# Kernel tuning notes

Measured on AMD Instinct MI355X. Metric: run time of the kernel, lower is better.

Reference implementation:

```python
import jax, jax.numpy as jnp
import numpy as np

B, T, D, I, C, H = 8192, 128, 7, 128, 10, 64
L = 2 ** D
SUBSET = int(I * 0.8)  # feature_subset_size = 102


def setup_inputs() -> dict:
    key = jax.random.key(0)
    ks = jax.random.split(key, 7)
    x = jax.random.normal(ks[0], (B, I), dtype=jnp.float32)
    # exact feature-subset mask: SUBSET ones per (tree, depth) row
    r = jax.random.uniform(ks[1], (T, D, I))
    ranks = jnp.argsort(jnp.argsort(r, axis=-1), axis=-1)
    feature_mask = (ranks < SUBSET).astype(jnp.float32)
    thresholds = jax.random.normal(ks[2], (T, D), dtype=jnp.float32)
    leaf_outputs = jax.random.normal(ks[3], (T, L, C), dtype=jnp.float32)
    W1 = jax.random.normal(ks[4], (I, H), dtype=jnp.float32) * 0.08
    b1 = jnp.zeros((H,), dtype=jnp.float32)
    W2 = jax.random.normal(ks[5], (H, T), dtype=jnp.float32) * 0.12
    b2 = jnp.zeros((T,), dtype=jnp.float32)
    return {"x": x, "feature_mask": feature_mask, "thresholds": thresholds,
            "leaf_outputs": leaf_outputs, "W1": W1, "b1": b1, "W2": W2, "b2": b2}


def reference(x, feature_mask, thresholds, leaf_outputs, W1, b1, W2, b2):
    depth = thresholds.shape[1]
    # split logits: masked feature sum minus threshold, per (batch, tree, depth)
    z = jnp.einsum('bi,tdi->btd', x, feature_mask) - thresholds[None, :, :]
    s = 0.5 * (z / (1.0 + jnp.abs(z)) + 1.0)  # scaled softsign split in (0,1)
    # probabilistic path routing: doubling concat, identical to torch loop
    p = jnp.ones((x.shape[0], feature_mask.shape[0], 1), dtype=x.dtype)
    for d in range(depth):
        sd = s[:, :, d:d + 1]            # [B, T, 1]
        p = jnp.concatenate([p * sd, p * (1.0 - sd)], axis=-1)  # [B, T, 2^(d+1)]
    leaf_probs = jax.nn.softmax(leaf_outputs, axis=-1)           # [T, L, C]
    tree_outputs = jnp.einsum('btl,tlc->btc', p, leaf_probs)     # [B, T, C]
    # instance-wise attention over trees (eval mode: no dropout)
    attn = jax.nn.softmax(jax.nn.relu(x @ W1 + b1) @ W2 + b2, axis=-1)  # [B, T]
    return jnp.sum(tree_outputs * attn[:, :, None], axis=1)     # [B, C]
```

## Files before the change

kernel.cpp:

```cpp
#include <hip/hip_runtime.h>
#include <hip/hip_bf16.h>
#include <hip/hip_fp16.h>


#define BB 8192
#define TT 128
#define II 128
#define CC 10
#define HH 64

typedef __attribute__((ext_vector_type(8))) short short8;
typedef __attribute__((ext_vector_type(16))) float floatx16;

static __device__ inline unsigned int pkbf(float lo, float hi) {
  __hip_bfloat162 h = __float22bfloat162_rn(make_float2(lo, hi));
  unsigned int u;
  __builtin_memcpy(&u, &h, 4);
  return u;
}

static __device__ inline unsigned int pkh(float lo, float hi) {
  __half2 h = __float22half2_rn(make_float2(lo, hi));
  unsigned int u;
  __builtin_memcpy(&u, &h, 4);
  return u;
}

static __device__ inline short8 cvt8(float4 a, float4 b) {
  union { short8 v; unsigned int u[4]; } r;
  r.u[0] = pkbf(a.x, a.y);
  r.u[1] = pkbf(a.z, a.w);
  r.u[2] = pkbf(b.x, b.y);
  r.u[3] = pkbf(b.z, b.w);
  return r.v;
}

__global__ __launch_bounds__(256, 2) void fused_kernel(
    const float* __restrict__ x, const float* __restrict__ mask,
    const float* __restrict__ thr, const float* __restrict__ lo,
    const float* __restrict__ W1, const float* __restrict__ b1,
    const float* __restrict__ W2, const float* __restrict__ b2,
    float* __restrict__ out) {
  __shared__ __align__(16) char smem_raw[63488];
  const int tid = threadIdx.x;
  const int wv = tid >> 6, lane = tid & 63;
  const int half = lane >> 5, l31 = lane & 31;
  const int tg = blockIdx.x >> 5;
  const int bg = blockIdx.x & 31;

  __half* zsl = (__half*)smem_raw;

  {
    const int m0 = tg * 56;
    short8 af0[8], af1[8];
    {
      const float* mrow0 = mask + (size_t)(m0 + l31) * II + half * 8;
      int mr1 = m0 + 28 + l31; if (mr1 > 895) mr1 = 895;
      const float* mrow1 = mask + (size_t)mr1 * II + half * 8;
#pragma unroll
      for (int s = 0; s < 8; ++s) {
        af0[s] = cvt8(*(const float4*)(mrow0 + s * 16),
                      *(const float4*)(mrow0 + s * 16 + 4));
        af1[s] = cvt8(*(const float4*)(mrow1 + s * 16),
                      *(const float4*)(mrow1 + s * 16 + 4));
      }
    }
    float th0[16], th1[16];
#pragma unroll
    for (int r = 0; r < 16; ++r) {
      int rw = (r & 3) + 8 * (r >> 2) + 4 * half;
      th0[r] = thr[m0 + rw];
      int m1 = m0 + 28 + rw;
      th1[r] = thr[m1 > 895 ? 895 : m1];
    }

#pragma unroll
    for (int nb = 0; nb < 2; ++nb) {
      const int nl = wv * 64 + nb * 32;
      const float* xrow = x + (size_t)(bg * 256 + nl + l31) * II + half * 8;
      short8 xf[8];
#pragma unroll
      for (int s = 0; s < 8; ++s)
        xf[s] = cvt8(*(const float4*)(xrow + s * 16),
                     *(const float4*)(xrow + s * 16 + 4));
      floatx16 acc0, acc1;
#pragma unroll
      for (int i = 0; i < 16; ++i) { acc0[i] = 0.f; acc1[i] = 0.f; }
#pragma unroll
      for (int s = 0; s < 8; ++s) {
        acc0 = __builtin_amdgcn_mfma_f32_32x32x16_bf16(af0[s], xf[s], acc0, 0, 0, 0);
        acc1 = __builtin_amdgcn_mfma_f32_32x32x16_bf16(af1[s], xf[s], acc1, 0, 0, 0);
      }
#pragma unroll
      for (int r = 0; r < 16; ++r) {
        int row = (r & 3) + 8 * (r >> 2) + 4 * half;
        if (row < 28) {
          int tl = row / 7;
          int d = row - tl * 7;
          float z = acc0[r] - th0[r];
          float o = 0.5f * (z / (1.f + fabsf(z)) + 1.f);
          zsl[(tl * 256 + nl + l31) * 8 + d] = __float2half(o);
          z = acc1[r] - th1[r];
          o = 0.5f * (z / (1.f + fabsf(z)) + 1.f);
          zsl[((tl + 4) * 256 + nl + l31) * 8 + d] = __float2half(o);
        }
      }
    }
  }

  {
    const int tsel = tg >> 2, lsel = tg & 3;
    __half* attnV = (__half*)(smem_raw + 59392);
    for (int p = 0; p < 2; ++p) {
      const int b0 = bg * 256 + p * 128 + wv * 32;

      short8 axf[8];
      const float* xrow = x + (size_t)(b0 + l31) * II + half * 8;
#pragma unroll
      for (int s = 0; s < 8; ++s)
        axf[s] = cvt8(*(const float4*)(xrow + s * 16),
                      *(const float4*)(xrow + s * 16 + 4));

      floatx16 acch[2];
#pragma unroll
      for (int i = 0; i < 16; ++i) { acch[0][i] = 0.f; acch[1][i] = 0.f; }
#pragma unroll
      for (int s = 0; s < 8; ++s) {
#pragma unroll
        for (int tile = 0; tile < 2; ++tile) {
          union { short8 v; unsigned int u[4]; } wf;
#pragma unroll
          for (int jp = 0; jp < 4; ++jp) {
            int k0 = s * 16 + half * 8 + jp * 2;
            float f0 = W1[(size_t)k0 * HH + tile * 32 + l31];
            float f1 = W1[(size_t)(k0 + 1) * HH + tile * 32 + l31];
            wf.u[jp] = pkbf(f0, f1);
          }
          acch[tile] = __builtin_amdgcn_mfma_f32_32x32x16_bf16(
              axf[s], wf.v, acch[tile], 0, 0, 0);
        }
      }
      __hip_bfloat16* hids = (__hip_bfloat16*)(smem_raw + 32768) + wv * (32 * 72);
#pragma unroll
      for (int tile = 0; tile < 2; ++tile) {
        float bh = b1[tile * 32 + l31];
#pragma unroll
        for (int r = 0; r < 16; ++r) {
          int row = (r & 3) + 8 * (r >> 2) + 4 * half;
          hids[row * 72 + tile * 32 + l31] =
              __float2bfloat16(fmaxf(acch[tile][r] + bh, 0.f));
        }
      }
      __syncthreads();

      short8 ahf[4];
#pragma unroll
      for (int s = 0; s < 4; ++s)
        ahf[s] = *(const short8*)(hids + l31 * 72 + s * 16 + half * 8);

      floatx16 accl[4];
#pragma unroll
      for (int tile = 0; tile < 4; ++tile) {
#pragma unroll
        for (int i = 0; i < 16; ++i) accl[tile][i] = 0.f;
#pragma unroll
        for (int s = 0; s < 4; ++s) {
          union { short8 v; unsigned int u[4]; } wf;
#pragma unroll
          for (int jp = 0; jp < 4; ++jp) {
            int k0 = s * 16 + half * 8 + jp * 2;
            float f0 = W2[(size_t)k0 * TT + tile * 32 + l31];
            float f1 = W2[(size_t)(k0 + 1) * TT + tile * 32 + l31];
            wf.u[jp] = pkbf(f0, f1);
          }
          accl[tile] = __builtin_amdgcn_mfma_f32_32x32x16_bf16(
              ahf[s], wf.v, accl[tile], 0, 0, 0);
        }
        float bt = b2[tile * 32 + l31];
#pragma unroll
        for (int i = 0; i < 16; ++i) accl[tile][i] += bt;
      }

      float mrow[16];
#pragma unroll
      for (int r = 0; r < 16; ++r)
        mrow[r] = fmaxf(fmaxf(accl[0][r], accl[1][r]),
                        fmaxf(accl[2][r], accl[3][r]));
#pragma unroll
      for (int msk = 1; msk <= 16; msk <<= 1)
#pragma unroll
        for (int r = 0; r < 16; ++r)
          mrow[r] = fmaxf(mrow[r], __shfl_xor(mrow[r], msk, 64));
      float srow[16];
#pragma unroll
      for (int r = 0; r < 16; ++r) srow[r] = 0.f;
#pragma unroll
      for (int tile = 0; tile < 4; ++tile)
#pragma unroll
        for (int r = 0; r < 16; ++r) {
          float e = __expf(accl[tile][r] - mrow[r]);
          accl[tile][r] = e;
          srow[r] += e;
        }
#pragma unroll
      for (int msk = 1; msk <= 16; msk <<= 1)
#pragma unroll
        for (int r = 0; r < 16; ++r)
          srow[r] += __shfl_xor(srow[r], msk, 64);
#pragma unroll
      for (int r = 0; r < 16; ++r) srow[r] = 1.f / srow[r];

#pragma unroll
      for (int tile = 0; tile < 4; ++tile) {
        if (tile == tsel) {
#pragma unroll
          for (int r = 0; r < 16; ++r) {
            int row = (r & 3) + 8 * (r >> 2) + 4 * half;
            if ((l31 >> 3) == lsel)
              attnV[(p * 128 + wv * 32 + row) * 8 + (l31 & 7)] =
                  __float2half(accl[tile][r] * srow[r]);
          }
        }
      }
      __syncthreads();
    }
  }

  {
    __half* lps = (__half*)(smem_raw + 53248);
    uint4* lpB = (uint4*)(smem_raw + 32768);
    for (int tt = 0; tt < 4; ++tt) {
      {
        int tl = tid >> 7, l = tid & 127;
        const float* row = lo + ((size_t)(tg * 8 + tt * 2 + tl) * 128 + l) * CC;
        float v[CC];
        float m = -1e30f;
#pragma unroll
        for (int c = 0; c < CC; ++c) { v[c] = row[c]; m = fmaxf(m, v[c]); }
        float s = 0.f;
#pragma unroll
        for (int c = 0; c < CC; ++c) { v[c] = __expf(v[c] - m); s += v[c]; }
        float inv = 1.f / s;
        __half* o = lps + (tl * 128 + l) * 12;
#pragma unroll
        for (int c = 0; c < CC; ++c) o[c] = __float2half(v[c] * inv);
      }
      __syncthreads();
#pragma unroll
      for (int jj = 0; jj < 4; ++jj) {
        int idx = tid + 256 * jj;
        int tl = idx >> 9, rem = idx & 511;
        int s = rem >> 6, ln = rem & 63;
        int hf = ln >> 5, n = ln & 31;
        if (n < CC) {
          unsigned int wd[4];
#pragma unroll
          for (int jp = 0; jp < 4; ++jp) {
            int l0 = s * 16 + hf * 8 + jp * 2;
            float f0 = __half2float(lps[(tl * 128 + l0) * 12 + n]);
            float f1 = __half2float(lps[(tl * 128 + l0 + 1) * 12 + n]);
            wd[jp] = pkh(f0, f1);
          }
          lpB[((tt * 2 + tl) * 8 + s) * 20 + n * 2 + hf] =
              make_uint4(wd[0], wd[1], wd[2], wd[3]);
        }
      }
      __syncthreads();
    }
  }

  {
    const uint4* zsl4 = (const uint4*)smem_raw;
    const uint4* lpB = (const uint4*)(smem_raw + 32768);
    const uint4* aV = (const uint4*)(smem_raw + 59392);
    const int bl = wv * 64 + l31;

    __half av0[8], av1[8];
    *(uint4*)av0 = aV[bl];
    *(uint4*)av1 = aV[bl + 32];

    floatx16 acc0, acc1;
#pragma unroll
    for (int i = 0; i < 16; ++i) { acc0[i] = 0.f; acc1[i] = 0.f; }

#pragma unroll
    for (int it = 0; it < 8; ++it) {
      uint4 sv0 = zsl4[it * 256 + bl];
      uint4 sv1 = zsl4[it * 256 + bl + 32];
      uint4 bf[8];
#pragma unroll
      for (int s = 0; s < 8; ++s)
        bf[s] = (l31 < CC) ? lpB[(it * 8 + s) * 20 + l31 * 2 + half]
                           : make_uint4(0u, 0u, 0u, 0u);

      __half2 pl2q[2][4];
      float wvq[2][8];
#pragma unroll
      for (int q = 0; q < 2; ++q) {
        const __half* sh = (const __half*)(q ? &sv1 : &sv0);
        float s0 = __half2float(sh[0]), s1 = __half2float(sh[1]);
        float s2 = __half2float(sh[2]), s3 = __half2float(sh[3]);
        float s4 = __half2float(sh[4]), s5 = __half2float(sh[5]);
        float s6 = __half2float(sh[6]);
        float A  = __half2float(q ? av1[it] : av0[it]);

        float s0c = 1.f - s0, s1c = 1.f - s1, s2c = 1.f - s2;
        float t0 = s0 * s1, t1 = s0c * s1, t2 = s0 * s1c, t3 = s0c * s1c;
        float pl[8];
        pl[0] = t0 * s2;  pl[1] = t1 * s2;  pl[2] = t2 * s2;  pl[3] = t3 * s2;
        pl[4] = t0 * s2c; pl[5] = t1 * s2c; pl[6] = t2 * s2c; pl[7] = t3 * s2c;
        float sel3 = half ? (1.f - s3) : s3;
        float Af = A * sel3;
        float s4c = 1.f - s4, s5c = 1.f - s5;
        float as6 = Af * s6, as6c = Af * (1.f - s6);
        float u0 = s4 * s5, u1 = s4c * s5, u2 = s4 * s5c, u3 = s4c * s5c;
        wvq[q][0] = u0 * as6;  wvq[q][1] = u1 * as6;
        wvq[q][2] = u2 * as6;  wvq[q][3] = u3 * as6;
        wvq[q][4] = u0 * as6c; wvq[q][5] = u1 * as6c;
        wvq[q][6] = u2 * as6c; wvq[q][7] = u3 * as6c;
#pragma unroll
        for (int jp = 0; jp < 4; ++jp)
          pl2q[q][jp] = __float22half2_rn(make_float2(pl[jp * 2], pl[jp * 2 + 1]));
      }

#pragma unroll
      for (int s = 0; s < 8; ++s) {
        union { short8 v; __half2 h[4]; } a0, a1;
        __half2 w20 = __half2half2(__float2half(wvq[0][s]));
        __half2 w21 = __half2half2(__float2half(wvq[1][s]));
#pragma unroll
        for (int jp = 0; jp < 4; ++jp) {
          a0.h[jp] = __hmul2(pl2q[0][jp], w20);
          a1.h[jp] = __hmul2(pl2q[1][jp], w21);
        }
        acc0 = __builtin_amdgcn_mfma_f32_32x32x16_f16(
            a0.v, *(const short8*)&bf[s], acc0, 0, 0, 0);
        acc1 = __builtin_amdgcn_mfma_f32_32x32x16_f16(
            a1.v, *(const short8*)&bf[s], acc1, 0, 0, 0);
      }
    }

    __syncthreads();
    float* red = (float*)(smem_raw + 32768);
    if (l31 < CC) {
#pragma unroll
      for (int r = 0; r < 16; ++r) {
        int row = (r & 3) + 8 * (r >> 2) + 4 * half;
        red[(wv * 64 + row) * 10 + l31] = acc0[r];
        red[(wv * 64 + 32 + row) * 10 + l31] = acc1[r];
      }
    }
    __syncthreads();
#pragma unroll
    for (int j = 0; j < 10; ++j) {
      int idx = tid + 256 * j;
      atomicAdd(out + (size_t)bg * 2560 + idx, red[idx]);
    }
  }
}

extern "C" void kernel_launch(void* const* d_in, const int* in_sizes, int n_in,
                              void* d_out, int out_size, void* d_ws, size_t ws_size,
                              hipStream_t stream) {
  const float* x    = (const float*)d_in[0];
  const float* mask = (const float*)d_in[1];
  const float* thr  = (const float*)d_in[2];
  const float* lo   = (const float*)d_in[3];
  const float* W1   = (const float*)d_in[4];
  const float* b1   = (const float*)d_in[5];
  const float* W2   = (const float*)d_in[6];
  const float* b2   = (const float*)d_in[7];
  float* out = (float*)d_out;

  hipMemsetAsync(out, 0, (size_t)out_size * sizeof(float), stream);
  fused_kernel<<<512, 256, 0, stream>>>(x, mask, thr, lo, W1, b1, W2, b2, out);
}
```

Baseline: 120.5 us.

## Split attention MLP and leaf softmax into a prep kernel to remove redundant work

Moves the attention MLP (x@W1, relu, @W2, softmax) and the leaf-output softmax/packing into a separate prep kernel that writes fp16 attention weights and packed leaf-probability B-fragments to workspace. Previously every block recomputed the full attention MLP for its batch rows and redid leaf softmax. The main kernel now reads these precomputed values and uses a finer grid (1024 blocks of 128 batch rows, 16 tree groups) with smaller shared memory to allow higher occupancy. The cost is an extra launch plus a global round trip for the attention and leaf data, and twice as many atomic-add blocks writing into the output.

```diff
diff --git a/kernel.cpp b/kernel.cpp
--- a/kernel.cpp
+++ b/kernel.cpp
@@ -8,6 +8,8 @@
 #define II 128
 #define CC 10
 #define HH 64
+
+#define OFF_LPB 524288
 
 typedef __attribute__((ext_vector_type(8))) short short8;
 typedef __attribute__((ext_vector_type(16))) float floatx16;
@@ -35,326 +37,304 @@
   return r.v;
 }
 
-__global__ __launch_bounds__(256, 2) void fused_kernel(
-    const float* __restrict__ x, const float* __restrict__ mask,
-    const float* __restrict__ thr, const float* __restrict__ lo,
+__global__ __launch_bounds__(256, 2) void prep_kernel(
+    const float* __restrict__ x, const float* __restrict__ lo,
     const float* __restrict__ W1, const float* __restrict__ b1,
     const float* __restrict__ W2, const float* __restrict__ b2,
-    float* __restrict__ out) {
-  __shared__ __align__(16) char smem_raw[63488];
+    __half* __restrict__ attnB, unsigned int* __restrict__ lpbG) {
+  __shared__ __align__(16) char smem_raw[18432];
+  const int blk = blockIdx.x;
   const int tid = threadIdx.x;
   const int wv = tid >> 6, lane = tid & 63;
   const int half = lane >> 5, l31 = lane & 31;
-  const int tg = blockIdx.x >> 5;
-  const int bg = blockIdx.x & 31;
+
+  if (blk < 64) {
+    const int b0 = blk * 128 + wv * 32;
+
+    short8 axf[8];
+    const float* xrow = x + (size_t)(b0 + l31) * II + half * 8;
+#pragma unroll
+    for (int s = 0; s < 8; ++s)
+      axf[s] = cvt8(*(const float4*)(xrow + s * 16),
+                    *(const float4*)(xrow + s * 16 + 4));
+
+    floatx16 acch[2];
+#pragma unroll
+    for (int i = 0; i < 16; ++i) { acch[0][i] = 0.f; acch[1][i] = 0.f; }
+#pragma unroll
+    for (int s = 0; s < 8; ++s) {
+#pragma unroll
+      for (int tile = 0; tile < 2; ++tile) {
+        union { short8 v; unsigned int u[4]; } wf;
+#pragma unroll
+        for (int jp = 0; jp < 4; ++jp) {
+          int k0 = s * 16 + half * 8 + jp * 2;
+          float f0 = W1[(size_t)k0 * HH + tile * 32 + l31];
+          float f1 = W1[(size_t)(k0 + 1) * HH + tile * 32 + l31];
+          wf.u[jp] = pkbf(f0, f1);
+        }
+        acch[tile] = __builtin_amdgcn_mfma_f32_32x32x16_bf16(
+            axf[s], wf.v, acch[tile], 0, 0, 0);
+      }
+    }
+    __hip_bfloat16* hids = (__hip_bfloat16*)smem_raw + wv * (32 * 72);
+#pragma unroll
+    for (int tile = 0; tile < 2; ++tile) {
+      float bh = b1[tile * 32 + l31];
+#pragma unroll
+      for (int r = 0; r < 16; ++r) {
+        int row = (r & 3) + 8 * (r >> 2) + 4 * half;
+        hids[row * 72 + tile * 32 + l31] =
+            __float2bfloat16(fmaxf(acch[tile][r] + bh, 0.f));
+      }
+    }
+    __syncthreads();
+
+    short8 ahf[4];
+#pragma unroll
+    for (int s = 0; s < 4; ++s)
+      ahf[s] = *(const short8*)(hids + l31 * 72 + s * 16 + half * 8);
+
+    floatx16 accl[4];
+#pragma unroll
+    for (int tile = 0; tile < 4; ++tile) {
+#pragma unroll
+      for (int i = 0; i < 16; ++i) accl[tile][i] = 0.f;
+#pragma unroll
+      for (int s = 0; s < 4; ++s) {
+        union { short8 v; unsigned int u[4]; } wf;
+#pragma unroll
+        for (int jp = 0; jp < 4; ++jp) {
+          int k0 = s * 16 + half * 8 + jp * 2;
+          float f0 = W2[(size_t)k0 * TT + tile * 32 + l31];
+          float f1 = W2[(size_t)(k0 + 1) * TT + tile * 32 + l31];
+          wf.u[jp] = pkbf(f0, f1);
+        }
+        accl[tile] = __builtin_amdgcn_mfma_f32_32x32x16_bf16(
+            ahf[s], wf.v, accl[tile], 0, 0, 0);
+      }
+      float bt = b2[tile * 32 + l31];
+#pragma unroll
+      for (int i = 0; i < 16; ++i) accl[tile][i] += bt;
+    }
+
+    float mrow[16];
+#pragma unroll
+    for (int r = 0; r < 16; ++r)
+      mrow[r] = fmaxf(fmaxf(accl[0][r], accl[1][r]),
+                      fmaxf(accl[2][r], accl[3][r]));
+#pragma unroll
+    for (int msk = 1; msk <= 16; msk <<= 1)
+#pragma unroll
+      for (int r = 0; r < 16; ++r)
+        mrow[r] = fmaxf(mrow[r], __shfl_xor(mrow[r], msk, 64));
+    float srow[16];
+#pragma unroll
+    for (int r = 0; r < 16; ++r) srow[r] = 0.f;
+#pragma unroll
+    for (int tile = 0; tile < 4; ++tile)
+#pragma unroll
+      for (int r = 0; r < 16; ++r) {
+        float e = __expf(accl[tile][r] - mrow[r]);
+        accl[tile][r] = e;
+        srow[r] += e;
+      }
+#pragma unroll
+    for (int msk = 1; msk <= 16; msk <<= 1)
+#pragma unroll
+      for (int r = 0; r < 16; ++r)
+        srow[r] += __shfl_xor(srow[r], msk, 64);
+#pragma unroll
+    for (int r = 0; r < 16; ++r) srow[r] = 1.f / srow[r];
+
+#pragma unroll
+    for (int tile = 0; tile < 4; ++tile)
+#pragma unroll
+      for (int r = 0; r < 16; ++r) {
+        int row = (r & 3) + 8 * (r >> 2) + 4 * half;
+        attnB[(size_t)(b0 + row) * TT + tile * 32 + l31] =
+            __float2half(accl[tile][r] * srow[r]);
+      }
+
+  } else {
+    float* lps = (float*)smem_raw;
+    const int t0 = (blk - 64) * 2;
+    {
+      int tl = tid >> 7, l = tid & 127;
+      const float* row = lo + ((size_t)(t0 + tl) * 128 + l) * CC;
+      float v[CC];
+      float m = -1e30f;
+#pragma unroll
+      for (int c = 0; c < CC; ++c) { v[c] = row[c]; m = fmaxf(m, v[c]); }
+      float s = 0.f;
+#pragma unroll
+      for (int c = 0; c < CC; ++c) { v[c] = __expf(v[c] - m); s += v[c]; }
+      float inv = 1.f / s;
+      float* o = lps + (tl * 128 + l) * 12;
+#pragma unroll
+      for (int c = 0; c < CC; ++c) o[c] = v[c] * inv;
+    }
+    __syncthreads();
+
+#pragma unroll
+    for (int jj = 0; jj < 2; ++jj) {
+      int idx = jj * 256 + tid;
+      if (idx < 320) {
+        int tl = idx / 160, rem = idx - tl * 160;
+        int s = rem / 20, e = rem - s * 20;
+        int n = e >> 1, hf = e & 1;
+        unsigned int wd[4];
+#pragma unroll
+        for (int jp = 0; jp < 4; ++jp) {
+          int l0 = s * 16 + hf * 8 + jp * 2;
+          float f0 = lps[(tl * 128 + l0) * 12 + n];
+          float f1 = lps[(tl * 128 + l0 + 1) * 12 + n];
+          wd[jp] = pkh(f0, f1);
+        }
+        ((uint4*)lpbG)[(size_t)(t0 + tl) * 160 + s * 20 + n * 2 + hf] =
+            make_uint4(wd[0], wd[1], wd[2], wd[3]);
+      }
+    }
+  }
+}
+
+__global__ __launch_bounds__(256, 4) void main_kernel(
+    const float* __restrict__ x, const float* __restrict__ mask,
+    const float* __restrict__ thr, const __half* __restrict__ attnB,
+    const unsigned int* __restrict__ lpbG, float* __restrict__ out) {
+  __shared__ __align__(16) char smem_raw[38912];
+  const int tid = threadIdx.x;
+  const int wv = tid >> 6, lane = tid & 63;
+  const int half = lane >> 5, l31 = lane & 31;
+  const int bg2 = blockIdx.x >> 4;
+  const int tg = blockIdx.x & 15;
 
   __half* zsl = (__half*)smem_raw;
+  uint4* attnV4 = (uint4*)(smem_raw + 16384);
+  uint4* lpB4 = (uint4*)(smem_raw + 18432);
+
+  if (tid < 128)
+    attnV4[tid] = ((const uint4*)attnB)[(size_t)(bg2 * 128 + tid) * 16 + tg];
+  {
+    const uint4* lg = (const uint4*)lpbG + (size_t)tg * 1280;
+#pragma unroll
+    for (int j = 0; j < 5; ++j) lpB4[j * 256 + tid] = lg[j * 256 + tid];
+  }
 
   {
     const int m0 = tg * 56;
-    short8 af0[8], af1[8];
-    {
-      const float* mrow0 = mask + (size_t)(m0 + l31) * II + half * 8;
-      int mr1 = m0 + 28 + l31; if (mr1 > 895) mr1 = 895;
-      const float* mrow1 = mask + (size_t)mr1 * II + half * 8;
-#pragma unroll
-      for (int s = 0; s < 8; ++s) {
-        af0[s] = cvt8(*(const float4*)(mrow0 + s * 16),
-                      *(const float4*)(mrow0 + s * 16 + 4));
-        af1[s] = cvt8(*(const float4*)(mrow1 + s * 16),
-                      *(const float4*)(mrow1 + s * 16 + 4));
-      }
-    }
-    float th0[16], th1[16];
-#pragma unroll
-    for (int r = 0; r < 16; ++r) {
-      int rw = (r & 3) + 8 * (r >> 2) + 4 * half;
-      th0[r] = thr[m0 + rw];
-      int m1 = m0 + 28 + rw;
-      th1[r] = thr[m1 > 895 ? 895 : m1];
-    }
-
-#pragma unroll
-    for (int nb = 0; nb < 2; ++nb) {
-      const int nl = wv * 64 + nb * 32;
-      const float* xrow = x + (size_t)(bg * 256 + nl + l31) * II + half * 8;
-      short8 xf[8];
+    short8 xf[8];
+    const float* xrow = x + (size_t)(bg2 * 128 + wv * 32 + l31) * II + half * 8;
+#pragma unroll
+    for (int s = 0; s < 8; ++s)
+      xf[s] = cvt8(*(const float4*)(xrow + s * 16),
+                   *(const float4*)(xrow + s * 16 + 4));
+
+#pragma unroll
+    for (int tile = 0; tile < 2; ++tile) {
+      int mr = m0 + tile * 28 + l31; if (mr > 895) mr = 895;
+      const float* mrow = mask + (size_t)mr * II + half * 8;
+      short8 af[8];
 #pragma unroll
       for (int s = 0; s < 8; ++s)
-        xf[s] = cvt8(*(const float4*)(xrow + s * 16),
-                     *(const float4*)(xrow + s * 16 + 4));
-      floatx16 acc0, acc1;
-#pragma unroll
-      for (int i = 0; i < 16; ++i) { acc0[i] = 0.f; acc1[i] = 0.f; }
-#pragma unroll
-      for (int s = 0; s < 8; ++s) {
-        acc0 = __builtin_amdgcn_mfma_f32_32x32x16_bf16(af0[s], xf[s], acc0, 0, 0, 0);
-        acc1 = __builtin_amdgcn_mfma_f32_32x32x16_bf16(af1[s], xf[s], acc1, 0, 0, 0);
-      }
+        af[s] = cvt8(*(const float4*)(mrow + s * 16),
+                     *(const float4*)(mrow + s * 16 + 4));
+      floatx16 acc;
+#pragma unroll
+      for (int i = 0; i < 16; ++i) acc[i] = 0.f;
+#pragma unroll
+      for (int s = 0; s < 8; ++s)
+        acc = __builtin_amdgcn_mfma_f32_32x32x16_bf16(af[s], xf[s], acc, 0, 0, 0);
+
 #pragma unroll
       for (int r = 0; r < 16; ++r) {
         int row = (r & 3) + 8 * (r >> 2) + 4 * half;
         if (row < 28) {
+          int mrr = m0 + tile * 28 + row;
+          float th = thr[mrr > 895 ? 895 : mrr];
           int tl = row / 7;
           int d = row - tl * 7;
-          float z = acc0[r] - th0[r];
+          float z = acc[r] - th;
           float o = 0.5f * (z / (1.f + fabsf(z)) + 1.f);
-          zsl[(tl * 256 + nl + l31) * 8 + d] = __float2half(o);
-          z = acc1[r] - th1[r];
-          o = 0.5f * (z / (1.f + fabsf(z)) + 1.f);
-          zsl[((tl + 4) * 256 + nl + l31) * 8 + d] = __float2half(o);
+          zsl[((tl + tile * 4) * 128 + wv * 32 + l31) * 8 + d] = __float2half(o);
         }
       }
     }
   }
-
-  {
-    const int tsel = tg >> 2, lsel = tg & 3;
-    __half* attnV = (__half*)(smem_raw + 59392);
-    for (int p = 0; p < 2; ++p) {
-      const int b0 = bg * 256 + p * 128 + wv * 32;
-
-      short8 axf[8];
-      const float* xrow = x + (size_t)(b0 + l31) * II + half * 8;
-#pragma unroll
-      for (int s = 0; s < 8; ++s)
-        axf[s] = cvt8(*(const float4*)(xrow + s * 16),
-                      *(const float4*)(xrow + s * 16 + 4));
-
-      floatx16 acch[2];
-#pragma unroll
-      for (int i = 0; i < 16; ++i) { acch[0][i] = 0.f; acch[1][i] = 0.f; }
-#pragma unroll
-      for (int s = 0; s < 8; ++s) {
-#pragma unroll
-        for (int tile = 0; tile < 2; ++tile) {
-          union { short8 v; unsigned int u[4]; } wf;
-#pragma unroll
-          for (int jp = 0; jp < 4; ++jp) {
-            int k0 = s * 16 + half * 8 + jp * 2;
-            float f0 = W1[(size_t)k0 * HH + tile * 32 + l31];
-            float f1 = W1[(size_t)(k0 + 1) * HH + tile * 32 + l31];
-            wf.u[jp] = pkbf(f0, f1);
-          }
-          acch[tile] = __builtin_amdgcn_mfma_f32_32x32x16_bf16(
-              axf[s], wf.v, acch[tile], 0, 0, 0);
-        }
-      }
-      __hip_bfloat16* hids = (__hip_bfloat16*)(smem_raw + 32768) + wv * (32 * 72);
-#pragma unroll
-      for (int tile = 0; tile < 2; ++tile) {
-        float bh = b1[tile * 32 + l31];
-#pragma unroll
-        for (int r = 0; r < 16; ++r) {
-          int row = (r & 3) + 8 * (r >> 2) + 4 * half;
-          hids[row * 72 + tile * 32 + l31] =
-              __float2bfloat16(fmaxf(acch[tile][r] + bh, 0.f));
-        }
-      }
-      __syncthreads();
-
-      short8 ahf[4];
-#pragma unroll
-      for (int s = 0; s < 4; ++s)
-        ahf[s] = *(const short8*)(hids + l31 * 72 + s * 16 + half * 8);
-
-      floatx16 accl[4];
-#pragma unroll
-      for (int tile = 0; tile < 4; ++tile) {
-#pragma unroll
-        for (int i = 0; i < 16; ++i) accl[tile][i] = 0.f;
-#pragma unroll
-        for (int s = 0; s < 4; ++s) {
-          union { short8 v; unsigned int u[4]; } wf;
-#pragma unroll
-          for (int jp = 0; jp < 4; ++jp) {
-            int k0 = s * 16 + half * 8 + jp * 2;
-            float f0 = W2[(size_t)k0 * TT + tile * 32 + l31];
-            float f1 = W2[(size_t)(k0 + 1) * TT + tile * 32 + l31];
-            wf.u[jp] = pkbf(f0, f1);
-          }
-          accl[tile] = __builtin_amdgcn_mfma_f32_32x32x16_bf16(
-              ahf[s], wf.v, accl[tile], 0, 0, 0);
-        }
-        float bt = b2[tile * 32 + l31];
-#pragma unroll
-        for (int i = 0; i < 16; ++i) accl[tile][i] += bt;
-      }
-
-      float mrow[16];
-#pragma unroll
-      for (int r = 0; r < 16; ++r)
-        mrow[r] = fmaxf(fmaxf(accl[0][r], accl[1][r]),
-                        fmaxf(accl[2][r], accl[3][r]));
-#pragma unroll
-      for (int msk = 1; msk <= 16; msk <<= 1)
-#pragma unroll
-        for (int r = 0; r < 16; ++r)
-          mrow[r] = fmaxf(mrow[r], __shfl_xor(mrow[r], msk, 64));
-      float srow[16];
-#pragma unroll
-      for (int r = 0; r < 16; ++r) srow[r] = 0.f;
-#pragma unroll
-      for (int tile = 0; tile < 4; ++tile)
-#pragma unroll
-        for (int r = 0; r < 16; ++r) {
-          float e = __expf(accl[tile][r] - mrow[r]);
-          accl[tile][r] = e;
-          srow[r] += e;
-        }
-#pragma unroll
-      for (int msk = 1; msk <= 16; msk <<= 1)
-#pragma unroll
-        for (int r = 0; r < 16; ++r)
-          srow[r] += __shfl_xor(srow[r], msk, 64);
-#pragma unroll
-      for (int r = 0; r < 16; ++r) srow[r] = 1.f / srow[r];
-
-#pragma unroll
-      for (int tile = 0; tile < 4; ++tile) {
-        if (tile == tsel) {
-#pragma unroll
-          for (int r = 0; r < 16; ++r) {
-            int row = (r & 3) + 8 * (r >> 2) + 4 * half;
-            if ((l31 >> 3) == lsel)
-              attnV[(p * 128 + wv * 32 + row) * 8 + (l31 & 7)] =
-                  __float2half(accl[tile][r] * srow[r]);
-          }
-        }
-      }
-      __syncthreads();
-    }
-  }
-
-  {
-    __half* lps = (__half*)(smem_raw + 53248);
-    uint4* lpB = (uint4*)(smem_raw + 32768);
-    for (int tt = 0; tt < 4; ++tt) {
-      {
-        int tl = tid >> 7, l = tid & 127;
-        const float* row = lo + ((size_t)(tg * 8 + tt * 2 + tl) * 128 + l) * CC;
-        float v[CC];
-        float m = -1e30f;
-#pragma unroll
-        for (int c = 0; c < CC; ++c) { v[c] = row[c]; m = fmaxf(m, v[c]); }
-        float s = 0.f;
-#pragma unroll
-        for (int c = 0; c < CC; ++c) { v[c] = __expf(v[c] - m); s += v[c]; }
-        float inv = 1.f / s;
-        __half* o = lps + (tl * 128 + l) * 12;
-#pragma unroll
-        for (int c = 0; c < CC; ++c) o[c] = __float2half(v[c] * inv);
-      }
-      __syncthreads();
-#pragma unroll
-      for (int jj = 0; jj < 4; ++jj) {
-        int idx = tid + 256 * jj;
-        int tl = idx >> 9, rem = idx & 511;
-        int s = rem >> 6, ln = rem & 63;
-        int hf = ln >> 5, n = ln & 31;
-        if (n < CC) {
-          unsigned int wd[4];
-#pragma unroll
-          for (int jp = 0; jp < 4; ++jp) {
-            int l0 = s * 16 + hf * 8 + jp * 2;
-            float f0 = __half2float(lps[(tl * 128 + l0) * 12 + n]);
-            float f1 = __half2float(lps[(tl * 128 + l0 + 1) * 12 + n]);
-            wd[jp] = pkh(f0, f1);
-          }
-          lpB[((tt * 2 + tl) * 8 + s) * 20 + n * 2 + hf] =
-              make_uint4(wd[0], wd[1], wd[2], wd[3]);
-        }
-      }
-      __syncthreads();
-    }
-  }
+  __syncthreads();
 
   {
     const uint4* zsl4 = (const uint4*)smem_raw;
-    const uint4* lpB = (const uint4*)(smem_raw + 32768);
-    const uint4* aV = (const uint4*)(smem_raw + 59392);
-    const int bl = wv * 64 + l31;
-
-    __half av0[8], av1[8];
-    *(uint4*)av0 = aV[bl];
-    *(uint4*)av1 = aV[bl + 32];
-
-    floatx16 acc0, acc1;
-#pragma unroll
-    for (int i = 0; i < 16; ++i) { acc0[i] = 0.f; acc1[i] = 0.f; }
+    const int bl = wv * 32 + l31;
+
+    __half av[8];
+    *(uint4*)av = attnV4[bl];
+
+    floatx16 acc;
+#pragma unroll
+    for (int i = 0; i < 16; ++i) acc[i] = 0.f;
 
 #pragma unroll
     for (int it = 0; it < 8; ++it) {
-      uint4 sv0 = zsl4[it * 256 + bl];
-      uint4 sv1 = zsl4[it * 256 + bl + 32];
+      uint4 sv = zsl4[it * 128 + bl];
       uint4 bf[8];
 #pragma unroll
       for (int s = 0; s < 8; ++s)
-        bf[s] = (l31 < CC) ? lpB[(it * 8 + s) * 20 + l31 * 2 + half]
+        bf[s] = (l31 < CC) ? lpB4[(it * 8 + s) * 20 + l31 * 2 + half]
                            : make_uint4(0u, 0u, 0u, 0u);
 
-      __half2 pl2q[2][4];
-      float wvq[2][8];
-#pragma unroll
-      for (int q = 0; q < 2; ++q) {
-        const __half* sh = (const __half*)(q ? &sv1 : &sv0);
-        float s0 = __half2float(sh[0]), s1 = __half2float(sh[1]);
-        float s2 = __half2float(sh[2]), s3 = __half2float(sh[3]);
-        float s4 = __half2float(sh[4]), s5 = __half2float(sh[5]);
-        float s6 = __half2float(sh[6]);
-        float A  = __half2float(q ? av1[it] : av0[it]);
-
-        float s0c = 1.f - s0, s1c = 1.f - s1, s2c = 1.f - s2;
-        float t0 = s0 * s1, t1 = s0c * s1, t2 = s0 * s1c, t3 = s0c * s1c;
-        float pl[8];
-        pl[0] = t0 * s2;  pl[1] = t1 * s2;  pl[2] = t2 * s2;  pl[3] = t3 * s2;
-        pl[4] = t0 * s2c; pl[5] = t1 * s2c; pl[6] = t2 * s2c; pl[7] = t3 * s2c;
-        float sel3 = half ? (1.f - s3) : s3;
-        float Af = A * sel3;
-        float s4c = 1.f - s4, s5c = 1.f - s5;
-        float as6 = Af * s6, as6c = Af * (1.f - s6);
-        float u0 = s4 * s5, u1 = s4c * s5, u2 = s4 * s5c, u3 = s4c * s5c;
-        wvq[q][0] = u0 * as6;  wvq[q][1] = u1 * as6;
-        wvq[q][2] = u2 * as6;  wvq[q][3] = u3 * as6;
-        wvq[q][4] = u0 * as6c; wvq[q][5] = u1 * as6c;
-        wvq[q][6] = u2 * as6c; wvq[q][7] = u3 * as6c;
-#pragma unroll
-        for (int jp = 0; jp < 4; ++jp)
-          pl2q[q][jp] = __float22half2_rn(make_float2(pl[jp * 2], pl[jp * 2 + 1]));
-      }
+      const __half* sh = (const __half*)&sv;
+      float s0 = __half2float(sh[0]), s1 = __half2float(sh[1]);
+      float s2 = __half2float(sh[2]), s3 = __half2float(sh[3]);
+      float s4 = __half2float(sh[4]), s5 = __half2float(sh[5]);
+      float s6 = __half2float(sh[6]);
+      float A  = __half2float(av[it]);
+
+      float s0c = 1.f - s0, s1c = 1.f - s1, s2c = 1.f - s2;
+      float t0 = s0 * s1, t1 = s0c * s1, t2 = s0 * s1c, t3 = s0c * s1c;
+      float pl[8];
+      pl[0] = t0 * s2;  pl[1] = t1 * s2;  pl[2] = t2 * s2;  pl[3] = t3 * s2;
+      pl[4] = t0 * s2c; pl[5] = t1 * s2c; pl[6] = t2 * s2c; pl[7] = t3 * s2c;
+      float sel3 = half ? (1.f - s3) : s3;
+      float Af = A * sel3;
+      float s4c = 1.f - s4, s5c = 1.f - s5;
+      float as6 = Af * s6, as6c = Af * (1.f - s6);
+      float u0 = s4 * s5, u1 = s4c * s5, u2 = s4 * s5c, u3 = s4c * s5c;
+      float wv8[8];
+      wv8[0] = u0 * as6;  wv8[1] = u1 * as6;
+      wv8[2] = u2 * as6;  wv8[3] = u3 * as6;
+      wv8[4] = u0 * as6c; wv8[5] = u1 * as6c;
+      wv8[6] = u2 * as6c; wv8[7] = u3 * as6c;
+      __half2 pl2[4];
+#pragma unroll
+      for (int jp = 0; jp < 4; ++jp)
+        pl2[jp] = __float22half2_rn(make_float2(pl[jp * 2], pl[jp * 2 + 1]));
 
 #pragma unroll
       for (int s = 0; s < 8; ++s) {
-        union { short8 v; __half2 h[4]; } a0, a1;
-        __half2 w20 = __half2half2(__float2half(wvq[0][s]));
-        __half2 w21 = __half2half2(__float2half(wvq[1][s]));
-#pragma unroll
-        for (int jp = 0; jp < 4; ++jp) {
-          a0.h[jp] = __hmul2(pl2q[0][jp], w20);
-          a1.h[jp] = __hmul2(pl2q[1][jp], w21);
-        }
-        acc0 = __builtin_amdgcn_mfma_f32_32x32x16_f16(
-            a0.v, *(const short8*)&bf[s], acc0, 0, 0, 0);
-        acc1 = __builtin_amdgcn_mfma_f32_32x32x16_f16(
-            a1.v, *(const short8*)&bf[s], acc1, 0, 0, 0);
+        union { short8 v; __half2 h[4]; } a0;
+        __half2 w2 = __half2half2(__float2half(wv8[s]));
+#pragma unroll
+        for (int jp = 0; jp < 4; ++jp) a0.h[jp] = __hmul2(pl2[jp], w2);
+        acc = __builtin_amdgcn_mfma_f32_32x32x16_f16(
+            a0.v, *(const short8*)&bf[s], acc, 0, 0, 0);
       }
     }
 
     __syncthreads();
-    float* red = (float*)(smem_raw + 32768);
+    float* red = (float*)(smem_raw + 18432);
     if (l31 < CC) {
 #pragma unroll
       for (int r = 0; r < 16; ++r) {
         int row = (r & 3) + 8 * (r >> 2) + 4 * half;
-        red[(wv * 64 + row) * 10 + l31] = acc0[r];
-        red[(wv * 64 + 32 + row) * 10 + l31] = acc1[r];
+        red[(wv * 32 + row) * 10 + l31] = acc[r];
       }
     }
     __syncthreads();
 #pragma unroll
-    for (int j = 0; j < 10; ++j) {
+    for (int j = 0; j < 5; ++j) {
       int idx = tid + 256 * j;
-      atomicAdd(out + (size_t)bg * 2560 + idx, red[idx]);
+      atomicAdd(out + (size_t)bg2 * 1280 + idx, red[idx]);
     }
   }
 }
@@ -371,7 +351,12 @@
   const float* W2   = (const float*)d_in[6];
   const float* b2   = (const float*)d_in[7];
   float* out = (float*)d_out;
+  float* ws  = (float*)d_ws;
+
+  __half*       attnB = (__half*)ws;
+  unsigned int* LPb   = (unsigned int*)(ws + OFF_LPB);
 
   hipMemsetAsync(out, 0, (size_t)out_size * sizeof(float), stream);
-  fused_kernel<<<512, 256, 0, stream>>>(x, mask, thr, lo, W1, b1, W2, b2, out);
-}
+  prep_kernel<<<128, 256, 0, stream>>>(x, lo, W1, b1, W2, b2, attnB, LPb);
+  main_kernel<<<1024, 256, 0, stream>>>(x, mask, thr, attnB, LPb, out);
+}
```

Result: faster. 117.4 us (-2.5%).
